# Optimization experiments

Hardware: AMD Instinct MI355X
Metric: run time of the kernel (lower is better)

Reference implementation:

```python
import jax, jax.numpy as jnp
import numpy as np

DEPTH = 10


def setup_inputs() -> dict:
    key = jax.random.key(0)
    k1, k2, k3, k4 = jax.random.split(key, 4)
    B, C_in, O, D, L = 4096, 512, 1024, DEPTH, 2 ** DEPTH
    x = jax.random.normal(k1, (B, C_in), dtype=jnp.float32)
    thresholds = 6.0 * jax.random.uniform(k2, (O, D), dtype=jnp.float32) - 3.0
    ordinals = jax.random.randint(k3, (O, D), 0, C_in, dtype=jnp.int64)
    weights = jax.random.normal(k4, (O, L), dtype=jnp.float32)
    return {"x": x, "thresholds": thresholds, "ordinals": ordinals, "weights": weights}


def reference(x, thresholds, ordinals, weights):
    # x: [B, C_in]; thresholds/ordinals: [O, D]; weights: [O, 2**D]
    O, D = thresholds.shape
    # Gather the D decision features for each fern: [B, O, D]
    feats = x[:, ordinals]
    margins = feats - thresholds[None, :, :]
    # Leaf index from sign bits (bit d is MSB-first): [B, O]
    powers = (2 ** (D - 1 - jnp.arange(D))).astype(jnp.int32)
    bits = (margins > 0).astype(jnp.int32)
    leaf = jnp.sum(bits * powers, axis=-1)
    # Hinge value: minimum absolute margin along the path: [B, O]
    min_margin = jnp.min(jnp.abs(margins), axis=-1)
    # Select leaf weight per (batch, fern): w[o, leaf[b, o]]
    w_sel = jnp.take_along_axis(weights[None, :, :], leaf[:, :, None], axis=2)[..., 0]
    return w_sel * min_margin  # [B, O]
```

## Files before the change

kernel.cpp:

```cpp
#include <hip/hip_runtime.h>


#define B_TOT   4096
#define CIN     512
#define O_TOT   1024
#define DEPTH   10
#define LEAVES  1024
#define OTILE   256
#define PAD     11

__global__ __launch_bounds__(256, 2) void fern_kernel(
    const float* __restrict__ x,
    const float* __restrict__ thresholds,
    const int*   __restrict__ ordinals,
    const float* __restrict__ weights,
    float*       __restrict__ out)
{
    __shared__ float xrow[CIN];
    __shared__ int   s_ord[OTILE * PAD];
    __shared__ float s_thr[OTILE * PAD];

    const int t  = threadIdx.x;
    const int b  = blockIdx.x;
    const int o0 = blockIdx.y * OTILE;

    const float2 xv = reinterpret_cast<const float2*>(x + (size_t)b * CIN)[t];
    reinterpret_cast<float2*>(xrow)[t] = xv;

    const int gbase = o0 * DEPTH;
#pragma unroll
    for (int k = 0; k < DEPTH; ++k) {
        const int j = k * OTILE + t;
        const int oo = j / DEPTH;
        const int dd = j - oo * DEPTH;
        s_ord[oo * PAD + dd] = ordinals[gbase + j];
        s_thr[oo * PAD + dd] = thresholds[gbase + j];
    }
    __syncthreads();

    const int o = o0 + t;
    int   leaf = 0;
    float mm   = 1e30f;
#pragma unroll
    for (int d = 0; d < DEPTH; ++d) {
        const int   ord    = s_ord[t * PAD + d];
        const float thr    = s_thr[t * PAD + d];
        const float margin = xrow[ord] - thr;
        leaf = (leaf << 1) | (margin > 0.0f ? 1 : 0);
        mm   = fminf(mm, fabsf(margin));
    }

    const float w = weights[(size_t)o * LEAVES + leaf];
    out[(size_t)b * O_TOT + o] = w * mm;
}

extern "C" void kernel_launch(void* const* d_in, const int* in_sizes, int n_in,
                              void* d_out, int out_size, void* d_ws, size_t ws_size,
                              hipStream_t stream) {
    const float* x          = (const float*)d_in[0];
    const float* thresholds = (const float*)d_in[1];
    const int*   ordinals   = (const int*)d_in[2];
    const float* weights    = (const float*)d_in[3];
    float*       out        = (float*)d_out;

    dim3 grid(B_TOT, O_TOT / OTILE);
    fern_kernel<<<grid, OTILE, 0, stream>>>(x, thresholds, ordinals, weights, out);
}
```

Measured before the change: 97.36 us.

## Tile batch rows per block to reuse fern ordinals and thresholds

Each block now handles eight batch rows instead of one. It stages an 8x512 slice of x in shared memory, loads each fern's ordinals and thresholds into registers once, and evaluates all eight rows with them. This cuts the cost of reloading ordinals and thresholds per row and reduces the block count. Output stores become nontemporal and the launch bound hint is raised to 4 blocks per CU. The costs are more shared memory per block and more registers per thread.

Result: faster. 88.26 us (-9.3%).

```diff
diff --git a/kernel.cpp b/kernel.cpp
--- a/kernel.cpp
+++ b/kernel.cpp
@@ -7,30 +7,38 @@
 #define DEPTH   10
 #define LEAVES  1024
 #define OTILE   256
+#define BTILE   8
 #define PAD     11
 
-__global__ __launch_bounds__(256, 2) void fern_kernel(
+__global__ __launch_bounds__(256, 4) void fern_kernel(
     const float* __restrict__ x,
     const float* __restrict__ thresholds,
     const int*   __restrict__ ordinals,
     const float* __restrict__ weights,
     float*       __restrict__ out)
 {
-    __shared__ float xrow[CIN];
+    __shared__ float xt[BTILE][CIN];
     __shared__ int   s_ord[OTILE * PAD];
     __shared__ float s_thr[OTILE * PAD];
 
     const int t  = threadIdx.x;
-    const int b  = blockIdx.x;
+    const int b0 = blockIdx.x * BTILE;
     const int o0 = blockIdx.y * OTILE;
 
-    const float2 xv = reinterpret_cast<const float2*>(x + (size_t)b * CIN)[t];
-    reinterpret_cast<float2*>(xrow)[t] = xv;
+#pragma unroll
+    for (int k = 0; k < 4; ++k) {
+        const int idx = k * 256 + t;
+        const int row = idx >> 7;
+        const int col = (idx & 127) << 2;
+        const float4 v = *reinterpret_cast<const float4*>(
+            x + (size_t)(b0 + row) * CIN + col);
+        *reinterpret_cast<float4*>(&xt[row][col]) = v;
+    }
 
     const int gbase = o0 * DEPTH;
 #pragma unroll
     for (int k = 0; k < DEPTH; ++k) {
-        const int j = k * OTILE + t;
+        const int j  = k * OTILE + t;
         const int oo = j / DEPTH;
         const int dd = j - oo * DEPTH;
         s_ord[oo * PAD + dd] = ordinals[gbase + j];
@@ -38,20 +46,30 @@
     }
     __syncthreads();
 
-    const int o = o0 + t;
-    int   leaf = 0;
-    float mm   = 1e30f;
+    int   ordr[DEPTH];
+    float thrr[DEPTH];
 #pragma unroll
     for (int d = 0; d < DEPTH; ++d) {
-        const int   ord    = s_ord[t * PAD + d];
-        const float thr    = s_thr[t * PAD + d];
-        const float margin = xrow[ord] - thr;
-        leaf = (leaf << 1) | (margin > 0.0f ? 1 : 0);
-        mm   = fminf(mm, fabsf(margin));
+        ordr[d] = s_ord[t * PAD + d];
+        thrr[d] = s_thr[t * PAD + d];
     }
 
-    const float w = weights[(size_t)o * LEAVES + leaf];
-    out[(size_t)b * O_TOT + o] = w * mm;
+    const int o = o0 + t;
+    const float* __restrict__ wrow = weights + (size_t)o * LEAVES;
+
+#pragma unroll
+    for (int bb = 0; bb < BTILE; ++bb) {
+        int   leaf = 0;
+        float mm   = 1e30f;
+#pragma unroll
+        for (int d = 0; d < DEPTH; ++d) {
+            const float margin = xt[bb][ordr[d]] - thrr[d];
+            leaf = (leaf << 1) | (margin > 0.0f ? 1 : 0);
+            mm   = fminf(mm, fabsf(margin));
+        }
+        const float w = wrow[leaf];
+        __builtin_nontemporal_store(w * mm, out + (size_t)(b0 + bb) * O_TOT + o);
+    }
 }
 
 extern "C" void kernel_launch(void* const* d_in, const int* in_sizes, int n_in,
@@ -63,6 +81,6 @@
     const float* weights    = (const float*)d_in[3];
     float*       out        = (float*)d_out;
 
-    dim3 grid(B_TOT, O_TOT / OTILE);
-    fern_kernel<<<grid, OTILE, 0, stream>>>(x, thresholds, ordinals, weights, out);
+    dim3 grid(B_TOT / BTILE, O_TOT / OTILE);
+    fern_kernel<<<grid, 256, 0, stream>>>(x, thresholds, ordinals, weights, out);
 }
```

## Tile over batch and ferns with transposed swizzled x in shared memory

Applied to the files above, without the earlier changes.

Each block now handles a 64x64 batch-by-fern tile instead of one batch row. The x rows are transposed into LDS with an XOR swizzle, lanes map to batch rows, and ordinals and thresholds become wave-uniform scalar loads. Outputs are staged in LDS and written back as coalesced vector nontemporal stores. The aim is to reuse x across 64 ferns, replace per-thread ordinal and threshold LDS traffic with scalar loads, and cut launch overhead. In exchange, the random weight gathers become scattered per lane across batch rows, and LDS use grows to 144 KB per block, which limits occupancy.

New measurement: 92.97 us. -4.5%, faster.

```diff
diff --git a/kernel.cpp b/kernel.cpp
--- a/kernel.cpp
+++ b/kernel.cpp
@@ -1,57 +1,85 @@
 #include <hip/hip_runtime.h>
 
 
-#define B_TOT   4096
-#define CIN     512
-#define O_TOT   1024
-#define DEPTH   10
-#define LEAVES  1024
-#define OTILE   256
-#define PAD     11
+#define B_TOT  4096
+#define CIN    512
+#define O_TOT  1024
+#define DEPTH  10
+#define LEAVES 1024
+#define BT     64
+#define OT     64
+#define NTHR   512
 
-__global__ __launch_bounds__(256, 2) void fern_kernel(
+typedef float vf4 __attribute__((ext_vector_type(4)));
+
+__global__ __launch_bounds__(NTHR, 2) void fern_kernel(
     const float* __restrict__ x,
     const float* __restrict__ thresholds,
     const int*   __restrict__ ordinals,
     const float* __restrict__ weights,
     float*       __restrict__ out)
 {
-    __shared__ float xrow[CIN];
-    __shared__ int   s_ord[OTILE * PAD];
-    __shared__ float s_thr[OTILE * PAD];
+    __shared__ float xT[CIN * BT];
+    __shared__ float osh[BT * OT];
 
-    const int t  = threadIdx.x;
-    const int b  = blockIdx.x;
-    const int o0 = blockIdx.y * OTILE;
+    const int t    = threadIdx.x;
+    const int lane = t & 63;
+    const int wu   = __builtin_amdgcn_readfirstlane(t >> 6);
+    const int b0   = blockIdx.x * BT;
+    const int o0   = blockIdx.y * OT;
 
-    const float2 xv = reinterpret_cast<const float2*>(x + (size_t)b * CIN)[t];
-    reinterpret_cast<float2*>(xrow)[t] = xv;
-
-    const int gbase = o0 * DEPTH;
 #pragma unroll
-    for (int k = 0; k < DEPTH; ++k) {
-        const int j = k * OTILE + t;
-        const int oo = j / DEPTH;
-        const int dd = j - oo * DEPTH;
-        s_ord[oo * PAD + dd] = ordinals[gbase + j];
-        s_thr[oo * PAD + dd] = thresholds[gbase + j];
+    for (int k = 0; k < 16; ++k) {
+        const int id = k * NTHR + t;
+        const int r  = id >> 7;
+        const int c4 = id & 127;
+        const vf4 v = *reinterpret_cast<const vf4*>(
+            x + (size_t)(b0 + r) * CIN + (c4 << 2));
+        const int rs   = r ^ (c4 & 31);
+        const int base = (c4 << 2) * BT + rs;
+        xT[base]          = v.x;
+        xT[base + BT]     = v.y;
+        xT[base + 2 * BT] = v.z;
+        xT[base + 3 * BT] = v.w;
     }
     __syncthreads();
 
-    const int o = o0 + t;
-    int   leaf = 0;
-    float mm   = 1e30f;
 #pragma unroll
-    for (int d = 0; d < DEPTH; ++d) {
-        const int   ord    = s_ord[t * PAD + d];
-        const float thr    = s_thr[t * PAD + d];
-        const float margin = xrow[ord] - thr;
-        leaf = (leaf << 1) | (margin > 0.0f ? 1 : 0);
-        mm   = fminf(mm, fabsf(margin));
+    for (int i = 0; i < 8; ++i) {
+        const int ol = wu * 8 + i;
+        const int o  = o0 + ol;
+        const int*   op = ordinals   + o * DEPTH;
+        const float* tp = thresholds + o * DEPTH;
+
+        int   leaf = 0;
+        float mm   = 1e30f;
+#pragma unroll
+        for (int d = 0; d < DEPTH; ++d) {
+            const int   ord = op[d];
+            const float thr = tp[d];
+            const float xv  = xT[ord * BT + (lane ^ ((ord >> 2) & 31))];
+            const float mg  = xv - thr;
+            leaf = (leaf << 1) | (mg > 0.0f ? 1 : 0);
+            mm   = fminf(mm, fabsf(mg));
+        }
+        const float wv = weights[(size_t)o * LEAVES + leaf];
+        osh[lane * OT + (ol ^ lane)] = wv * mm;
     }
+    __syncthreads();
 
-    const float w = weights[(size_t)o * LEAVES + leaf];
-    out[(size_t)b * O_TOT + o] = w * mm;
+    const int rb = t >> 3;
+#pragma unroll
+    for (int k = 0; k < 2; ++k) {
+        const int g  = (t & 7) + (k << 3);
+        const int ob = g << 2;
+        vf4 v;
+        v.x = osh[rb * OT + ((ob + 0) ^ rb)];
+        v.y = osh[rb * OT + ((ob + 1) ^ rb)];
+        v.z = osh[rb * OT + ((ob + 2) ^ rb)];
+        v.w = osh[rb * OT + ((ob + 3) ^ rb)];
+        __builtin_nontemporal_store(v, reinterpret_cast<vf4*>(
+            out + (size_t)(b0 + rb) * O_TOT + o0 + ob));
+    }
 }
 
 extern "C" void kernel_launch(void* const* d_in, const int* in_sizes, int n_in,
@@ -63,6 +91,6 @@
     const float* weights    = (const float*)d_in[3];
     float*       out        = (float*)d_out;
 
-    dim3 grid(B_TOT, O_TOT / OTILE);
-    fern_kernel<<<grid, OTILE, 0, stream>>>(x, thresholds, ordinals, weights, out);
+    dim3 grid(B_TOT / BT, O_TOT / OT);
+    fern_kernel<<<grid, NTHR, 0, stream>>>(x, thresholds, ordinals, weights, out);
 }
```
